# Kernel optimization log

Hardware: AMD Instinct MI355X
Metric: run time of the kernel (lower is better)

Reference implementation:

```python
import jax, jax.numpy as jnp
import numpy as np

B, S, D = 8, 2048, 512

def setup_inputs() -> dict:
    key = jax.random.key(0)
    k1, k2 = jax.random.split(key)
    lstm_out = jax.random.normal(k1, (B, S, D), dtype=jnp.float32)
    # xavier_uniform init for [D, D]
    limit = float(np.sqrt(6.0 / (D + D)))
    attention_weights = jax.random.uniform(k2, (D, D), dtype=jnp.float32, minval=-limit, maxval=limit)
    return {"lstm_out": lstm_out, "attention_weights": attention_weights}

def reference(lstm_out, attention_weights):
    # scores[b,i,j] = tanh( (x W) x^T )
    proj = jnp.einsum('bsd,de->bse', lstm_out, attention_weights)          # [B,S,D]
    scores = jnp.tanh(jnp.einsum('bsd,btd->bst', proj, lstm_out))          # [B,S,S]
    attn = jax.nn.softmax(scores, axis=-1)                                 # [B,S,S]
    return jnp.einsum('bst,btd->bsd', attn, lstm_out)                      # [B,S,D]
```

## Files before the change

### kernel.cpp

```cpp
#include <hip/hip_runtime.h>
#include <hip/hip_bf16.h>

typedef __bf16 bf16;
typedef __attribute__((ext_vector_type(8))) __bf16 bf16x8;
typedef __attribute__((ext_vector_type(4))) float floatx4;

#define NPART 16
#define NSLOT 32

__device__ __forceinline__ void gl_lds16(const bf16* g, bf16* l) {
    __builtin_amdgcn_global_load_lds(
        (const __attribute__((address_space(1))) unsigned int*)g,
        (__attribute__((address_space(3))) unsigned int*)l,
        16, 0, 0);
}

__device__ __forceinline__ void swizzle_mn(int& bm, int& bn) {
    int gx = gridDim.x;
    int f  = blockIdx.y * gx + blockIdx.x;
    int st = f >> 3, r = f & 7;
    int mgroups = gx >> 2;
    bm = (st % mgroups) * 4 + (r & 3);
    bn = (st / mgroups) * 2 + (r >> 2);
}

__global__ __launch_bounds__(256) void cast_both(const float* __restrict__ in,
                                                 bf16* __restrict__ outn,
                                                 bf16* __restrict__ outt,
                                                 int R, int C) {
    __shared__ float tile[32][33];
    const long long bz = blockIdx.z;
    in   += bz * (long long)R * C;
    outn += bz * (long long)R * C;
    outt += bz * (long long)R * C;
    const int r0 = blockIdx.x * 32, c0 = blockIdx.y * 32;
    const int tx = threadIdx.x & 31, ty = threadIdx.x >> 5;
#pragma unroll
    for (int i = 0; i < 32; i += 8) {
        float v = in[(long long)(r0 + ty + i) * C + (c0 + tx)];
        tile[ty + i][tx] = v;
        outn[(long long)(r0 + ty + i) * C + (c0 + tx)] = (bf16)v;
    }
    __syncthreads();
#pragma unroll
    for (int i = 0; i < 32; i += 8)
        outt[(long long)(c0 + ty + i) * R + (r0 + tx)] = (bf16)tile[tx][ty + i];
}

__global__ __launch_bounds__(256) void cast_transpose(const float* __restrict__ in,
                                                      bf16* __restrict__ out,
                                                      int R, int C) {
    __shared__ float tile[32][33];
    const int r0 = blockIdx.x * 32, c0 = blockIdx.y * 32;
    const int tx = threadIdx.x & 31, ty = threadIdx.x >> 5;
#pragma unroll
    for (int i = 0; i < 32; i += 8)
        tile[ty + i][tx] = in[(long long)(r0 + ty + i) * C + (c0 + tx)];
    __syncthreads();
#pragma unroll
    for (int i = 0; i < 32; i += 8)
        out[(long long)(c0 + ty + i) * R + (r0 + tx)] = (bf16)tile[tx][ty + i];
}

__device__ __forceinline__ float fast_tanh(float v) {
    float e = __expf(2.0f * v);
    return 1.0f - 2.0f / (e + 1.0f);
}

template <int MODE>
__global__ __launch_bounds__(512) void gemm256(const bf16* __restrict__ A,
                                               const bf16* __restrict__ Bm,
                                               void* __restrict__ Cout,
                                               float* __restrict__ rpart,
                                               int M, int N, int K,
                                               long long batchA, long long batchB,
                                               long long batchC, long long batchR) {
    const long long bz = blockIdx.z;
    A  += bz * batchA;
    Bm += bz * batchB;

    __shared__ bf16 As[3][256 * 64];
    __shared__ bf16 Bs[3][128 * 64];
    __shared__ float rs[256];

    const int t    = threadIdx.x;
    const int lane = t & 63;
    const int wid  = t >> 6;
    const int quad = lane >> 4;
    const int l16  = lane & 15;
    const int wr   = wid >> 1;
    const int wc   = wid & 1;

    int bm, bn;
    swizzle_mn(bm, bn);
    const int m0 = bm * 256;
    const int n0 = bn * 128;

    floatx4 acc[4][4] = {};

    const int ra  = t >> 3;
    const int ca8 = (((t & 7) ^ (ra & 7))) * 8;
    const long long rstep = 64LL * K;
    const bf16* Abase = A + (long long)(m0 + ra) * K + ca8;
    const bf16* Bbase = Bm + (long long)(n0 + ra) * K + ca8;

    if (MODE == 2) {
        if (t < 256) {
            const float* pp = rpart + (bz * batchR + m0 + t) * NSLOT;
            float s = 0.f;
#pragma unroll
            for (int c = 0; c < NSLOT / 4; ++c) {
                float4 p = ((const float4*)pp)[c];
                s += (p.x + p.y) + (p.z + p.w);
            }
            rs[t] = 1.0f / s;
        }
    }

    const int NT = K >> 6;

    auto stage = [&](int buf, int kt) {
        const long long k0 = (long long)kt * 64;
#pragma unroll
        for (int i = 0; i < 4; ++i)
            gl_lds16(Abase + k0 + i * rstep, &As[buf][(t + 512 * i) * 8]);
#pragma unroll
        for (int i = 0; i < 2; ++i)
            gl_lds16(Bbase + k0 + i * rstep, &Bs[buf][(t + 512 * i) * 8]);
    };

    auto compute = [&](int buf) {
#pragma unroll
        for (int s = 0; s < 2; ++s) {
            const int cq = ((s * 4 + quad) ^ (l16 & 7)) * 8;
            bf16x8 af[4], bfr[4];
#pragma unroll
            for (int i = 0; i < 4; ++i)
                af[i] = *(const bf16x8*)(&As[buf][(wr * 64 + i * 16 + l16) * 64 + cq]);
#pragma unroll
            for (int j = 0; j < 4; ++j)
                bfr[j] = *(const bf16x8*)(&Bs[buf][(wc * 64 + j * 16 + l16) * 64 + cq]);
            __builtin_amdgcn_s_setprio(1);
#pragma unroll
            for (int i = 0; i < 4; ++i)
#pragma unroll
                for (int j = 0; j < 4; ++j)
                    acc[i][j] = __builtin_amdgcn_mfma_f32_16x16x32_bf16(af[i], bfr[j], acc[i][j], 0, 0, 0);
            __builtin_amdgcn_s_setprio(0);
        }
    };

    stage(0, 0);
    stage(1, 1);
    asm volatile("s_waitcnt vmcnt(6)\n\ts_barrier" ::: "memory");

    for (int kt = 0; kt < NT - 1; ++kt) {
        if (kt + 2 < NT) {
            stage((kt + 2) % 3, kt + 2);
            compute(kt % 3);
            asm volatile("s_waitcnt vmcnt(6)\n\ts_barrier" ::: "memory");
        } else {
            compute(kt % 3);
            asm volatile("s_waitcnt vmcnt(0)\n\ts_barrier" ::: "memory");
        }
    }
    compute((NT - 1) % 3);

    if (MODE == 1) {
        bf16* Cg = (bf16*)Cout + bz * batchC;
        const int slot = bn * 2 + wc;
#pragma unroll
        for (int i = 0; i < 4; ++i)
#pragma unroll
            for (int r = 0; r < 4; ++r) {
                long long row = m0 + wr * 64 + i * 16 + quad * 4 + r;
                float s = 0.f;
#pragma unroll
                for (int j = 0; j < 4; ++j) {
                    float v = __expf(fast_tanh(acc[i][j][r]));
                    s += v;
                    Cg[row * (long long)N + (n0 + wc * 64 + j * 16 + l16)] = (bf16)v;
                }
#pragma unroll
                for (int msk = 1; msk < 16; msk <<= 1) s += __shfl_xor(s, msk);
                if (l16 == 0)
                    rpart[(bz * batchR + row) * NSLOT + slot] = s;
            }
    } else {
        float* Og = (float*)Cout + bz * batchC;
#pragma unroll
        for (int i = 0; i < 4; ++i)
#pragma unroll
            for (int r = 0; r < 4; ++r) {
                int rl = wr * 64 + i * 16 + quad * 4 + r;
                float inv = rs[rl];
                long long row = m0 + rl;
#pragma unroll
                for (int j = 0; j < 4; ++j)
                    Og[row * (long long)N + (n0 + wc * 64 + j * 16 + l16)] = acc[i][j][r] * inv;
            }
    }
}

__global__ __launch_bounds__(256) void gemm64_nt(const bf16* __restrict__ A,
                                                 const bf16* __restrict__ Bm,
                                                 bf16* __restrict__ Cout,
                                                 int M, int N, int K) {
    __shared__ bf16 As[2][64 * 64];
    __shared__ bf16 Bs[2][128 * 64];

    const int t    = threadIdx.x;
    const int lane = t & 63;
    const int wave = t >> 6;
    const int quad = lane >> 4;
    const int l16  = lane & 15;

    const int m0 = blockIdx.x * 64;
    const int n0 = blockIdx.y * 128;
    const int wn = wave * 32;

    floatx4 acc[4][2] = {};

    const int ra = t >> 3;
    const int ca = (((t & 7) ^ (ra & 7))) * 8;
    const long long rstep = 32LL * K;
    const bf16* Abase = A + (long long)(m0 + ra) * K + ca;
    const bf16* Bbase = Bm + (long long)(n0 + ra) * K + ca;

    const int cq0 = ((quad) ^ (l16 & 7)) * 8;
    const int cq1 = ((4 + quad) ^ (l16 & 7)) * 8;

    auto stage = [&](int buf, int k0) {
#pragma unroll
        for (int i = 0; i < 2; ++i)
            gl_lds16(Abase + k0 + i * rstep, &As[buf][(t + 256 * i) * 8]);
#pragma unroll
        for (int i = 0; i < 4; ++i)
            gl_lds16(Bbase + k0 + i * rstep, &Bs[buf][(t + 256 * i) * 8]);
    };

    auto compute = [&](int buf) {
#pragma unroll
        for (int s = 0; s < 2; ++s) {
            const int cq = s ? cq1 : cq0;
            bf16x8 af[4], bfr[2];
#pragma unroll
            for (int i = 0; i < 4; ++i)
                af[i] = *(const bf16x8*)(&As[buf][(i * 16 + l16) * 64 + cq]);
#pragma unroll
            for (int j = 0; j < 2; ++j)
                bfr[j] = *(const bf16x8*)(&Bs[buf][(wn + j * 16 + l16) * 64 + cq]);
#pragma unroll
            for (int i = 0; i < 4; ++i)
#pragma unroll
                for (int j = 0; j < 2; ++j)
                    acc[i][j] = __builtin_amdgcn_mfma_f32_16x16x32_bf16(af[i], bfr[j], acc[i][j], 0, 0, 0);
        }
    };

    stage(0, 0);
    __syncthreads();

    for (int k0 = 0; k0 < K; k0 += 128) {
        if (k0 + 64 < K) stage(1, k0 + 64);
        compute(0);
        __syncthreads();
        if (k0 + 128 < K) stage(0, k0 + 128);
        compute(1);
        __syncthreads();
    }

#pragma unroll
    for (int i = 0; i < 4; ++i)
#pragma unroll
        for (int r = 0; r < 4; ++r) {
            long long row = m0 + i * 16 + quad * 4 + r;
#pragma unroll
            for (int j = 0; j < 2; ++j)
                Cout[row * (long long)N + (n0 + wn + j * 16 + l16)] = (bf16)acc[i][j][r];
        }
}

extern "C" void kernel_launch(void* const* d_in, const int* in_sizes, int n_in,
                              void* d_out, int out_size, void* d_ws, size_t ws_size,
                              hipStream_t stream) {
    const int B = 8, S = 2048, D = 512;
    const float* x = (const float*)d_in[0];
    const float* W = (const float*)d_in[1];
    float* out = (float*)d_out;

    const size_t nx = (size_t)B * S * D;
    const size_t nw = (size_t)D * D;

    char* ws = (char*)d_ws;
    auto al = [](size_t v) { return (v + 255) & ~(size_t)255; };
    size_t off = 0;
    bf16* xb = (bf16*)(ws + off); off = al(off + nx * 2);
    bf16* xt = (bf16*)(ws + off); off = al(off + nx * 2);
    bf16* pb = (bf16*)(ws + off); off = al(off + nx * 2);
    bf16* wt = (bf16*)(ws + off); off = al(off + nw * 2);
    float* rpart = (float*)(ws + off); off = al(off + (size_t)B * S * NSLOT * 4);
    bf16* sb = (bf16*)(ws + off);
    const size_t full_need = off + (size_t)B * S * S * 2;
    const bool batched = (ws_size >= full_need);

    { dim3 g(S / 32, D / 32, B); cast_both<<<g, 256, 0, stream>>>(x, xb, xt, S, D); }
    { dim3 g(D / 32, D / 32, 1); cast_transpose<<<g, 256, 0, stream>>>(W, wt, D, D); }

    {
        dim3 g(B * S / 64, D / 128, 1);
        gemm64_nt<<<g, 256, 0, stream>>>(xb, wt, pb, B * S, D, D);
    }

    const long long sd = (long long)S * D;
    const long long ss = (long long)S * S;

    if (batched) {
        dim3 g2(S / 256, S / 128, B);
        gemm256<1><<<g2, 512, 0, stream>>>(pb, xb, (void*)sb, rpart, S, S, D, sd, sd, ss, S);
        dim3 g4(S / 256, D / 128, B);
        gemm256<2><<<g4, 512, 0, stream>>>(sb, xt, (void*)out, rpart, S, D, S, ss, sd, sd, S);
    } else {
        for (int b = 0; b < B; ++b) {
            dim3 g2(S / 256, S / 128, 1);
            gemm256<1><<<g2, 512, 0, stream>>>(pb + (size_t)b * sd, xb + (size_t)b * sd,
                                               (void*)sb, rpart + (size_t)b * S * NSLOT,
                                               S, S, D, 0, 0, 0, S);
            dim3 g4(S / 256, D / 128, 1);
            gemm256<2><<<g4, 512, 0, stream>>>(sb, xt + (size_t)b * sd,
                                               (void*)(out + (size_t)b * sd), rpart + (size_t)b * S * NSLOT,
                                               S, D, S, 0, 0, 0, S);
        }
    }
}
```

Measured before the change: 234.3 us.

## Split GEMM template into specialized scores/PV kernels with half-K double-buffered pipeline

Replaces the templated triple-buffered gemm256 with two specialized kernels that have compile-time K/N. Both use a double-buffered LDS layout split into 32-wide K halves, with loads of the next half issued between MFMA phases and explicit barriers. The scores kernel grows its tile to 256x256 with a 2x4 wave grid and two accumulator sets, raising reuse per loaded byte. The cost is more registers and barriers, plus a hand-counted vmcnt schedule that may be fragile.

```diff
diff --git a/kernel.cpp b/kernel.cpp
--- a/kernel.cpp
+++ b/kernel.cpp
@@ -5,8 +5,9 @@
 typedef __attribute__((ext_vector_type(8))) __bf16 bf16x8;
 typedef __attribute__((ext_vector_type(4))) float floatx4;
 
-#define NPART 16
 #define NSLOT 32
+
+#define BARM() asm volatile("s_barrier" ::: "memory")
 
 __device__ __forceinline__ void gl_lds16(const bf16* g, bf16* l) {
     __builtin_amdgcn_global_load_lds(
@@ -67,139 +68,254 @@
     return 1.0f - 2.0f / (e + 1.0f);
 }
 
-template <int MODE>
-__global__ __launch_bounds__(512) void gemm256(const bf16* __restrict__ A,
-                                               const bf16* __restrict__ Bm,
-                                               void* __restrict__ Cout,
-                                               float* __restrict__ rpart,
-                                               int M, int N, int K,
-                                               long long batchA, long long batchB,
-                                               long long batchC, long long batchR) {
+
+__global__ __launch_bounds__(512) void gemm_scores(const bf16* __restrict__ A,
+                                                   const bf16* __restrict__ Bm,
+                                                   bf16* __restrict__ Cout,
+                                                   float* __restrict__ rpart,
+                                                   long long batchA, long long batchB,
+                                                   long long batchC, long long batchR) {
+    constexpr int K = 512, NT = K / 64, N = 2048;
+    __shared__ bf16 As[32768];
+    __shared__ bf16 Bs[32768];
+
     const long long bz = blockIdx.z;
     A  += bz * batchA;
     Bm += bz * batchB;
 
-    __shared__ bf16 As[3][256 * 64];
-    __shared__ bf16 Bs[3][128 * 64];
+    const int t = threadIdx.x, lane = t & 63, w = t >> 6;
+    const int quad = lane >> 4, l16 = lane & 15;
+    const int wr = w >> 2, wc = w & 3;
+    int bm, bn; swizzle_mn(bm, bn);
+    const int m0 = bm * 256, n0 = bn * 256;
+
+    const int gch = ((lane & 3) ^ ((lane >> 3) & 3)) * 8;
+    const bf16* aSrc = A  + (long long)(m0 + w * 32 + (lane >> 2)) * K + gch;
+    const bf16* bSrc = Bm + (long long)(n0 + w * 32 + (lane >> 2)) * K + gch;
+    const int ldst = w * 1024 + lane * 8;
+    const long long j16K = 16LL * K;
+    const int rdch = (quad ^ ((l16 >> 1) & 3)) * 8;
+    const int rA0 = (wr * 128 + l16) * 32 + rdch;
+    const int rB0 = (wc * 64 + l16) * 32 + rdch;
+
+    floatx4 accL[4][4] = {}, accH[4][4] = {};
+    bf16x8 af[4], bfr[4];
+
+    auto stgA = [&](int kt, int h, int buf) {
+        const bf16* s = aSrc + (long long)kt * 64 + h * 32;
+        bf16* d = &As[(buf * 2 + h) * 8192 + ldst];
+        gl_lds16(s, d); gl_lds16(s + j16K, d + 512);
+    };
+    auto stgB = [&](int kt, int h, int buf) {
+        const bf16* s = bSrc + (long long)kt * 64 + h * 32;
+        bf16* d = &Bs[(buf * 2 + h) * 8192 + ldst];
+        gl_lds16(s, d); gl_lds16(s + j16K, d + 512);
+    };
+    auto rdB4 = [&](int p, int h) {
+#pragma unroll
+        for (int j = 0; j < 4; ++j)
+            bfr[j] = *(const bf16x8*)&Bs[(p * 2 + h) * 8192 + rB0 + j * 512];
+    };
+    auto rdA4 = [&](int p, int h, int mh) {
+#pragma unroll
+        for (int i = 0; i < 4; ++i)
+            af[i] = *(const bf16x8*)&As[(p * 2 + h) * 8192 + rA0 + mh * 2048 + i * 512];
+    };
+    auto mmL = [&]() {
+        __builtin_amdgcn_s_setprio(1);
+#pragma unroll
+        for (int i = 0; i < 4; ++i)
+#pragma unroll
+            for (int j = 0; j < 4; ++j)
+                accL[i][j] = __builtin_amdgcn_mfma_f32_16x16x32_bf16(af[i], bfr[j], accL[i][j], 0, 0, 0);
+        __builtin_amdgcn_s_setprio(0);
+    };
+    auto mmH = [&]() {
+        __builtin_amdgcn_s_setprio(1);
+#pragma unroll
+        for (int i = 0; i < 4; ++i)
+#pragma unroll
+            for (int j = 0; j < 4; ++j)
+                accH[i][j] = __builtin_amdgcn_mfma_f32_16x16x32_bf16(af[i], bfr[j], accH[i][j], 0, 0, 0);
+        __builtin_amdgcn_s_setprio(0);
+    };
+
+    stgA(0, 0, 0); stgB(0, 0, 0); stgA(0, 1, 0); stgB(0, 1, 0); stgA(1, 0, 1); stgB(1, 0, 1);
+    asm volatile("s_waitcnt vmcnt(8)" ::: "memory"); BARM();
+
+    for (int kt = 0; kt < NT - 2; ++kt) {
+        const int p = kt & 1, q = p ^ 1;
+        rdB4(p, 0); rdA4(p, 0, 0); stgA(kt + 1, 1, q);
+        BARM(); mmL(); BARM();
+        rdA4(p, 0, 1); stgB(kt + 1, 1, q);
+        BARM(); mmH();
+        asm volatile("s_waitcnt vmcnt(8) lgkmcnt(0)" ::: "memory"); BARM();
+        rdB4(p, 1); rdA4(p, 1, 0); stgA(kt + 2, 0, p);
+        BARM(); mmL(); BARM();
+        rdA4(p, 1, 1); stgB(kt + 2, 0, p);
+        BARM(); mmH();
+        asm volatile("s_waitcnt vmcnt(8) lgkmcnt(0)" ::: "memory"); BARM();
+    }
+    {
+        const int p = (NT - 2) & 1, q = p ^ 1;
+        rdB4(p, 0); rdA4(p, 0, 0); stgA(NT - 1, 1, q);
+        BARM(); mmL(); BARM();
+        rdA4(p, 0, 1); stgB(NT - 1, 1, q);
+        BARM(); mmH();
+        asm volatile("s_waitcnt vmcnt(8) lgkmcnt(0)" ::: "memory"); BARM();
+        rdB4(p, 1); rdA4(p, 1, 0);
+        BARM(); mmL(); BARM();
+        rdA4(p, 1, 1);
+        BARM(); mmH();
+        asm volatile("s_waitcnt vmcnt(4) lgkmcnt(0)" ::: "memory"); BARM();
+    }
+    {
+        const int p = (NT - 1) & 1;
+        rdB4(p, 0); rdA4(p, 0, 0);
+        BARM(); mmL(); BARM();
+        rdA4(p, 0, 1);
+        BARM(); mmH();
+        asm volatile("s_waitcnt vmcnt(0) lgkmcnt(0)" ::: "memory"); BARM();
+        rdB4(p, 1); rdA4(p, 1, 0);
+        BARM(); mmL(); BARM();
+        rdA4(p, 1, 1);
+        BARM(); mmH();
+    }
+
+    bf16* Cg = Cout + bz * batchC;
+    const int slot = bn * 4 + wc;
+#define EPI(ACC, MH)                                                                  \
+    _Pragma("unroll") for (int i = 0; i < 4; ++i)                                     \
+    _Pragma("unroll") for (int r = 0; r < 4; ++r) {                                   \
+        long long row = m0 + wr * 128 + (MH) * 64 + i * 16 + quad * 4 + r;            \
+        float s = 0.f;                                                                \
+        _Pragma("unroll") for (int j = 0; j < 4; ++j) {                               \
+            float v = __expf(fast_tanh(ACC[i][j][r]));                                \
+            s += v;                                                                   \
+            Cg[row * (long long)N + (n0 + wc * 64 + j * 16 + l16)] = (bf16)v;         \
+        }                                                                             \
+        _Pragma("unroll") for (int msk = 1; msk < 16; msk <<= 1) s += __shfl_xor(s, msk); \
+        if (l16 == 0) rpart[(bz * batchR + row) * NSLOT + slot] = s;                  \
+    }
+    EPI(accL, 0)
+    EPI(accH, 1)
+#undef EPI
+}
+
+__global__ __launch_bounds__(512) void gemm_pv(const bf16* __restrict__ A,
+                                               const bf16* __restrict__ Bm,
+                                               float* __restrict__ Out,
+                                               const float* __restrict__ rpart,
+                                               long long batchA, long long batchB,
+                                               long long batchC, long long batchR) {
+    constexpr int K = 2048, NT = K / 64, N = 512;
+    __shared__ bf16 As[32768];
+    __shared__ bf16 Bs[16384];
     __shared__ float rs[256];
 
-    const int t    = threadIdx.x;
-    const int lane = t & 63;
-    const int wid  = t >> 6;
-    const int quad = lane >> 4;
-    const int l16  = lane & 15;
-    const int wr   = wid >> 1;
-    const int wc   = wid & 1;
-
-    int bm, bn;
-    swizzle_mn(bm, bn);
-    const int m0 = bm * 256;
-    const int n0 = bn * 128;
+    const long long bz = blockIdx.z;
+    A  += bz * batchA;
+    Bm += bz * batchB;
+
+    const int t = threadIdx.x, lane = t & 63, w = t >> 6;
+    const int quad = lane >> 4, l16 = lane & 15;
+    const int wr = w >> 1, wc = w & 1;
+    int bm, bn; swizzle_mn(bm, bn);
+    const int m0 = bm * 256, n0 = bn * 128;
+
+    if (t < 256) {
+        const float* pp = rpart + (bz * batchR + m0 + t) * NSLOT;
+        float s = 0.f;
+#pragma unroll
+        for (int c = 0; c < NSLOT / 4; ++c) {
+            float4 p4 = ((const float4*)pp)[c];
+            s += (p4.x + p4.y) + (p4.z + p4.w);
+        }
+        rs[t] = 1.0f / s;
+    }
+    asm volatile("" ::: "memory");
+
+    const int gch = ((lane & 3) ^ ((lane >> 3) & 3)) * 8;
+    const bf16* aSrc = A  + (long long)(m0 + w * 32 + (lane >> 2)) * K + gch;
+    const bf16* bSrc = Bm + (long long)(n0 + w * 16 + (lane >> 2)) * K + gch;
+    const int ldstA = w * 1024 + lane * 8;
+    const int ldstB = w * 512 + lane * 8;
+    const long long j16K = 16LL * K;
+    const int rdch = (quad ^ ((l16 >> 1) & 3)) * 8;
+    const int rA0 = (wr * 64 + l16) * 32 + rdch;
+    const int rB0 = (wc * 64 + l16) * 32 + rdch;
 
     floatx4 acc[4][4] = {};
-
-    const int ra  = t >> 3;
-    const int ca8 = (((t & 7) ^ (ra & 7))) * 8;
-    const long long rstep = 64LL * K;
-    const bf16* Abase = A + (long long)(m0 + ra) * K + ca8;
-    const bf16* Bbase = Bm + (long long)(n0 + ra) * K + ca8;
-
-    if (MODE == 2) {
-        if (t < 256) {
-            const float* pp = rpart + (bz * batchR + m0 + t) * NSLOT;
-            float s = 0.f;
-#pragma unroll
-            for (int c = 0; c < NSLOT / 4; ++c) {
-                float4 p = ((const float4*)pp)[c];
-                s += (p.x + p.y) + (p.z + p.w);
-            }
-            rs[t] = 1.0f / s;
+    bf16x8 af[4], bfr[4];
+
+    auto stgA = [&](int kt, int h, int buf) {
+        const bf16* s = aSrc + (long long)kt * 64 + h * 32;
+        bf16* d = &As[(buf * 2 + h) * 8192 + ldstA];
+        gl_lds16(s, d); gl_lds16(s + j16K, d + 512);
+    };
+    auto stgB = [&](int kt, int h, int buf) {
+        gl_lds16(bSrc + (long long)kt * 64 + h * 32, &Bs[(buf * 2 + h) * 4096 + ldstB]);
+    };
+    auto rd8 = [&](int p, int h) {
+#pragma unroll
+        for (int i = 0; i < 4; ++i)
+            af[i] = *(const bf16x8*)&As[(p * 2 + h) * 8192 + rA0 + i * 512];
+#pragma unroll
+        for (int j = 0; j < 4; ++j)
+            bfr[j] = *(const bf16x8*)&Bs[(p * 2 + h) * 4096 + rB0 + j * 512];
+    };
+    auto mm16 = [&]() {
+        __builtin_amdgcn_s_setprio(1);
+#pragma unroll
+        for (int i = 0; i < 4; ++i)
+#pragma unroll
+            for (int j = 0; j < 4; ++j)
+                acc[i][j] = __builtin_amdgcn_mfma_f32_16x16x32_bf16(af[i], bfr[j], acc[i][j], 0, 0, 0);
+        __builtin_amdgcn_s_setprio(0);
+    };
+
+    stgA(0, 0, 0); stgB(0, 0, 0); stgA(0, 1, 0); stgB(0, 1, 0); stgA(1, 0, 1); stgB(1, 0, 1);
+    asm volatile("s_waitcnt vmcnt(3)" ::: "memory"); BARM();
+
+    for (int kt = 0; kt < NT - 2; ++kt) {
+        const int p = kt & 1, q = p ^ 1;
+        rd8(p, 0); stgA(kt + 1, 1, q); stgB(kt + 1, 1, q);
+        BARM(); mm16();
+        asm volatile("s_waitcnt vmcnt(6) lgkmcnt(0)" ::: "memory"); BARM();
+        rd8(p, 1); stgA(kt + 2, 0, p); stgB(kt + 2, 0, p);
+        BARM(); mm16();
+        asm volatile("s_waitcnt vmcnt(6) lgkmcnt(0)" ::: "memory"); BARM();
+    }
+    {
+        const int p = (NT - 2) & 1, q = p ^ 1;
+        rd8(p, 0); stgA(NT - 1, 1, q); stgB(NT - 1, 1, q);
+        BARM(); mm16();
+        asm volatile("s_waitcnt vmcnt(6) lgkmcnt(0)" ::: "memory"); BARM();
+        rd8(p, 1);
+        BARM(); mm16();
+        asm volatile("s_waitcnt vmcnt(3) lgkmcnt(0)" ::: "memory"); BARM();
+    }
+    {
+        const int p = (NT - 1) & 1;
+        rd8(p, 0);
+        BARM(); mm16();
+        asm volatile("s_waitcnt vmcnt(0) lgkmcnt(0)" ::: "memory"); BARM();
+        rd8(p, 1);
+        BARM(); mm16();
+    }
+
+    float* Og = Out + bz * batchC;
+#pragma unroll
+    for (int i = 0; i < 4; ++i)
+#pragma unroll
+        for (int r = 0; r < 4; ++r) {
+            int rl = wr * 64 + i * 16 + quad * 4 + r;
+            float inv = rs[rl];
+            long long row = m0 + rl;
+#pragma unroll
+            for (int j = 0; j < 4; ++j)
+                Og[row * (long long)N + (n0 + wc * 64 + j * 16 + l16)] = acc[i][j][r] * inv;
         }
-    }
-
-    const int NT = K >> 6;
-
-    auto stage = [&](int buf, int kt) {
-        const long long k0 = (long long)kt * 64;
-#pragma unroll
-        for (int i = 0; i < 4; ++i)
-            gl_lds16(Abase + k0 + i * rstep, &As[buf][(t + 512 * i) * 8]);
-#pragma unroll
-        for (int i = 0; i < 2; ++i)
-            gl_lds16(Bbase + k0 + i * rstep, &Bs[buf][(t + 512 * i) * 8]);
-    };
-
-    auto compute = [&](int buf) {
-#pragma unroll
-        for (int s = 0; s < 2; ++s) {
-            const int cq = ((s * 4 + quad) ^ (l16 & 7)) * 8;
-            bf16x8 af[4], bfr[4];
-#pragma unroll
-            for (int i = 0; i < 4; ++i)
-                af[i] = *(const bf16x8*)(&As[buf][(wr * 64 + i * 16 + l16) * 64 + cq]);
-#pragma unroll
-            for (int j = 0; j < 4; ++j)
-                bfr[j] = *(const bf16x8*)(&Bs[buf][(wc * 64 + j * 16 + l16) * 64 + cq]);
-            __builtin_amdgcn_s_setprio(1);
-#pragma unroll
-            for (int i = 0; i < 4; ++i)
-#pragma unroll
-                for (int j = 0; j < 4; ++j)
-                    acc[i][j] = __builtin_amdgcn_mfma_f32_16x16x32_bf16(af[i], bfr[j], acc[i][j], 0, 0, 0);
-            __builtin_amdgcn_s_setprio(0);
-        }
-    };
-
-    stage(0, 0);
-    stage(1, 1);
-    asm volatile("s_waitcnt vmcnt(6)\n\ts_barrier" ::: "memory");
-
-    for (int kt = 0; kt < NT - 1; ++kt) {
-        if (kt + 2 < NT) {
-            stage((kt + 2) % 3, kt + 2);
-            compute(kt % 3);
-            asm volatile("s_waitcnt vmcnt(6)\n\ts_barrier" ::: "memory");
-        } else {
-            compute(kt % 3);
-            asm volatile("s_waitcnt vmcnt(0)\n\ts_barrier" ::: "memory");
-        }
-    }
-    compute((NT - 1) % 3);
-
-    if (MODE == 1) {
-        bf16* Cg = (bf16*)Cout + bz * batchC;
-        const int slot = bn * 2 + wc;
-#pragma unroll
-        for (int i = 0; i < 4; ++i)
-#pragma unroll
-            for (int r = 0; r < 4; ++r) {
-                long long row = m0 + wr * 64 + i * 16 + quad * 4 + r;
-                float s = 0.f;
-#pragma unroll
-                for (int j = 0; j < 4; ++j) {
-                    float v = __expf(fast_tanh(acc[i][j][r]));
-                    s += v;
-                    Cg[row * (long long)N + (n0 + wc * 64 + j * 16 + l16)] = (bf16)v;
-                }
-#pragma unroll
-                for (int msk = 1; msk < 16; msk <<= 1) s += __shfl_xor(s, msk);
-                if (l16 == 0)
-                    rpart[(bz * batchR + row) * NSLOT + slot] = s;
-            }
-    } else {
-        float* Og = (float*)Cout + bz * batchC;
-#pragma unroll
-        for (int i = 0; i < 4; ++i)
-#pragma unroll
-            for (int r = 0; r < 4; ++r) {
-                int rl = wr * 64 + i * 16 + quad * 4 + r;
-                float inv = rs[rl];
-                long long row = m0 + rl;
-#pragma unroll
-                for (int j = 0; j < 4; ++j)
-                    Og[row * (long long)N + (n0 + wc * 64 + j * 16 + l16)] = acc[i][j][r] * inv;
-            }
-    }
 }
 
 __global__ __launch_bounds__(256) void gemm64_nt(const bf16* __restrict__ A,
@@ -316,20 +432,19 @@
     const long long ss = (long long)S * S;
 
     if (batched) {
-        dim3 g2(S / 256, S / 128, B);
-        gemm256<1><<<g2, 512, 0, stream>>>(pb, xb, (void*)sb, rpart, S, S, D, sd, sd, ss, S);
+        dim3 g2(S / 256, S / 256, B);
+        gemm_scores<<<g2, 512, 0, stream>>>(pb, xb, sb, rpart, sd, sd, ss, S);
         dim3 g4(S / 256, D / 128, B);
-        gemm256<2><<<g4, 512, 0, stream>>>(sb, xt, (void*)out, rpart, S, D, S, ss, sd, sd, S);
+        gemm_pv<<<g4, 512, 0, stream>>>(sb, xt, out, rpart, ss, sd, sd, S);
     } else {
         for (int b = 0; b < B; ++b) {
-            dim3 g2(S / 256, S / 128, 1);
-            gemm256<1><<<g2, 512, 0, stream>>>(pb + (size_t)b * sd, xb + (size_t)b * sd,
-                                               (void*)sb, rpart + (size_t)b * S * NSLOT,
-                                               S, S, D, 0, 0, 0, S);
+            dim3 g2(S / 256, S / 256, 1);
+            gemm_scores<<<g2, 512, 0, stream>>>(pb + (size_t)b * sd, xb + (size_t)b * sd,
+                                                sb, rpart + (size_t)b * S * NSLOT, 0, 0, 0, S);
             dim3 g4(S / 256, D / 128, 1);
-            gemm256<2><<<g4, 512, 0, stream>>>(sb, xt + (size_t)b * sd,
-                                               (void*)(out + (size_t)b * sd), rpart + (size_t)b * S * NSLOT,
-                                               S, D, S, 0, 0, 0, S);
+            gemm_pv<<<g4, 512, 0, stream>>>(sb, xt + (size_t)b * sd,
+                                            out + (size_t)b * sd, rpart + (size_t)b * S * NSLOT,
+                                            0, 0, 0, S);
         }
     }
 }
```

Result: faster. 214.0 us (-8.7%).
